# Kernel tuning notes

Hardware: AMD Instinct MI355X
Metric: run time of the kernel (lower is better)

Reference implementation:

```python
import jax, jax.numpy as jnp
import numpy as np

D_MODEL = 768
D_FF = 3072
N_BEHAVIORS = 4
EPS = 1e-12


def layer_norm(x, g, b):
    m = jnp.mean(x, axis=-1, keepdims=True)
    v = jnp.mean(jnp.square(x - m), axis=-1, keepdims=True)
    return (x - m) * jax.lax.rsqrt(v + EPS) * g + b


def setup_inputs() -> dict:
    key = jax.random.key(0)
    ks = jax.random.split(key, 8)
    B, L = 8, 2048
    s1 = 1.0 / np.sqrt(D_MODEL)
    s2 = 1.0 / np.sqrt(D_FF)
    return {
        "input_tensor": jax.random.normal(ks[0], (B, L, D_MODEL), dtype=jnp.float32),
        "type_seq": jax.random.randint(ks[1], (B, L), 0, N_BEHAVIORS + 1),
        # per-behavior FeedForward params, stacked on leading n dim
        "W1": jax.random.normal(ks[2], (N_BEHAVIORS, D_MODEL, D_FF), dtype=jnp.float32) * s1,
        "b1": jnp.zeros((N_BEHAVIORS, D_FF), dtype=jnp.float32),
        "W2": jax.random.normal(ks[3], (N_BEHAVIORS, D_FF, D_MODEL), dtype=jnp.float32) * s2,
        "b2": jnp.zeros((N_BEHAVIORS, D_MODEL), dtype=jnp.float32),
        "ln_g": jnp.ones((N_BEHAVIORS, D_MODEL), dtype=jnp.float32),
        "ln_b": jnp.zeros((N_BEHAVIORS, D_MODEL), dtype=jnp.float32),
        # outer LayerNorm params
        "out_g": jnp.ones((D_MODEL,), dtype=jnp.float32),
        "out_b": jnp.zeros((D_MODEL,), dtype=jnp.float32),
    }


def reference(input_tensor, type_seq, W1, b1, W2, b2, ln_g, ln_b, out_g, out_b):
    n = W1.shape[0]
    # run every behavior's FeedForward over the full sequence (dense over-compute)
    h = jnp.einsum('BLH,nHF->nBLF', input_tensor, W1) + b1[:, None, None, :]
    h = jax.nn.gelu(h, approximate=False)  # torch 'gelu' = exact erf form
    h = jnp.einsum('nBLF,nFH->nBLH', h, W2) + b2[:, None, None, :]
    # per-expert residual LayerNorm (FeedForward with residual=True)
    h = layer_norm(h + input_tensor[None], ln_g[:, None, None, :], ln_b[:, None, None, :])
    # prepend zeros branch (class 0 = padding) then one-hot select per token
    stacked = jnp.concatenate([jnp.zeros_like(input_tensor)[None], h], axis=0)  # [n+1,B,L,H]
    onehot = jax.nn.one_hot(type_seq, n + 1, dtype=input_tensor.dtype)  # [B,L,n+1]
    sel = jnp.einsum('nBLH,BLn->BLH', stacked, onehot)
    # dropout is identity in eval; fused residual + LayerNorm
    return layer_norm(sel + input_tensor, out_g, out_b)
```

## Files before the change

### kernel.cpp

```cpp
#include <hip/hip_runtime.h>
#include <hip/hip_bf16.h>
#include <math.h>

#define NTOK   16384
#define DM     768
#define DF     3072
#define NEXP   4

#define RBLKS  64
#define XBLKS  768
#define WBLKS  288
#define PREP_BLKS (RBLKS + XBLKS + 2 * WBLKS)

typedef short bf16x8 __attribute__((ext_vector_type(8)));
typedef float f32x4  __attribute__((ext_vector_type(4)));

#define WS_CNT    0u
#define WS_BASES  256u
#define WS_POS    512u
#define WS_LIST   (512u + 65536u)
#define WS_XB     (WS_LIST + 262144u)
#define WS_W1T    (WS_XB + 25165824u)
#define WS_W2T    (WS_W1T + 18874368u)
#define WS_H1     (WS_W2T + 18874368u)
#define WS_H2     (WS_H1 + 100663296u)
#define WS_END    (WS_H2 + 25165824u)

__device__ __forceinline__ ushort f2bf(float f) {
    unsigned int v; __builtin_memcpy(&v, &f, 4);
    v = v + 0x7fffu + ((v >> 16) & 1u);
    return (ushort)(v >> 16);
}
__device__ __forceinline__ float bf2f(ushort u) {
    unsigned int v = ((unsigned int)u) << 16;
    float f; __builtin_memcpy(&f, &v, 4); return f;
}

__device__ __forceinline__ float fast_gelu(float v) {
    float y = v + 0.044715f * v * v * v;
    float e = __builtin_amdgcn_exp2f(-2.3022082f * y);
    return v * __builtin_amdgcn_rcpf(1.0f + e);
}

typedef __attribute__((address_space(1))) const void gvoid_t;
typedef __attribute__((address_space(3))) void lvoid_t;
__device__ __forceinline__ void cp16(const void* g, void* l) {
    __builtin_amdgcn_global_load_lds((gvoid_t*)g, (lvoid_t*)l, 16, 0, 0);
}

__device__ __forceinline__ int xcd_remap(int id, int T) {
    const int q = T >> 3, r = T & 7;
    const int x = id & 7, j = id >> 3;
    return (x < r ? x * (q + 1) : r * (q + 1) + (x - r) * q) + j;
}

__device__ __forceinline__ void transpose_tile(
    const float* __restrict__ src, ushort* __restrict__ dst, int R, int C,
    int bx, int by, int tid, ushort* tile ) {
    const int r0 = by * 64, c0 = bx * 64;
#pragma unroll
    for (int q = 0; q < 2; ++q) {
        int li = q * 256 + tid;
        int r = li >> 3, c = (li & 7) * 8;
        const float* s = src + (size_t)(r0 + r) * C + (c0 + c);
        float4 v0 = *(const float4*)s;
        float4 v1 = *(const float4*)(s + 4);
        ushort tmp[8];
        tmp[0] = f2bf(v0.x); tmp[1] = f2bf(v0.y); tmp[2] = f2bf(v0.z); tmp[3] = f2bf(v0.w);
        tmp[4] = f2bf(v1.x); tmp[5] = f2bf(v1.y); tmp[6] = f2bf(v1.z); tmp[7] = f2bf(v1.w);
        int sw = (((c >> 3) ^ ((r >> 3) & 7)) << 3);
        *(uint4*)&tile[r * 72 + sw] = *(uint4*)tmp;
    }
    __syncthreads();
#pragma unroll
    for (int q = 0; q < 2; ++q) {
        int li = q * 256 + tid;
        int r = li >> 3, c = (li & 7) * 8;
        ushort tmp[8];
#pragma unroll
        for (int j = 0; j < 8; ++j)
            tmp[j] = tile[(c + j) * 72 +
                          ((((r >> 3) & 7) ^ (((c + j) >> 3) & 7)) << 3) + (r & 7)];
        *(uint4*)(dst + (size_t)(c0 + r) * R + (r0 + c)) = *(uint4*)tmp;
    }
}

__global__ __launch_bounds__(256) void prep_kernel(
    const int* __restrict__ type_seq, const float* __restrict__ X,
    const float* __restrict__ W1, const float* __restrict__ W2,
    int* __restrict__ cnt,
    int* __restrict__ pos_of, int* __restrict__ list,
    ushort* __restrict__ Xb, ushort* __restrict__ W1t, ushort* __restrict__ W2t) {
    __shared__ ushort tile[64 * 72];
    __shared__ int lcnt[NEXP];
    __shared__ int lbase[NEXP];
    const int tid = threadIdx.x;
    const int bid = blockIdx.x;

    if (bid < RBLKS) {
        if (tid < NEXP) lcnt[tid] = 0;
        __syncthreads();
        const int lane = tid & 63;
        const int t = bid * 256 + tid;
        const int k = type_seq[t];
        int my_e = -1, my_p = 0;
#pragma unroll
        for (int e = 0; e < NEXP; ++e) {
            unsigned long long m = __ballot(k == e + 1);
            int total = __popcll(m);
            int b = 0;
            if (lane == 0 && total) b = atomicAdd(&lcnt[e], total);
            b = __shfl(b, 0, 64);
            if (k == e + 1) {
                my_e = e;
                my_p = b + __popcll(m & ((1ull << lane) - 1ull));
            }
        }
        __syncthreads();
        if (tid < NEXP && lcnt[tid] > 0)
            lbase[tid] = atomicAdd(&cnt[tid], lcnt[tid]);
        __syncthreads();
        if (my_e >= 0) {
            int gp = lbase[my_e] + my_p;
            list[my_e * NTOK + gp] = t;
            pos_of[t] = gp;
        }
        return;
    }

    int id = bid - RBLKS;
    if (id < XBLKS) {
        size_t ibase = ((size_t)id * 8 * 256 + tid) * 8;
        float4 va[8], vb[8];
#pragma unroll
        for (int k = 0; k < 8; ++k) {
            va[k] = *(const float4*)(X + ibase + (size_t)k * 2048);
            vb[k] = *(const float4*)(X + ibase + (size_t)k * 2048 + 4);
        }
#pragma unroll
        for (int k = 0; k < 8; ++k) {
            ushort tmp[8];
            tmp[0] = f2bf(va[k].x); tmp[1] = f2bf(va[k].y);
            tmp[2] = f2bf(va[k].z); tmp[3] = f2bf(va[k].w);
            tmp[4] = f2bf(vb[k].x); tmp[5] = f2bf(vb[k].y);
            tmp[6] = f2bf(vb[k].z); tmp[7] = f2bf(vb[k].w);
            *(uint4*)(Xb + ibase + (size_t)k * 2048) = *(uint4*)tmp;
        }
        return;
    }
    id -= XBLKS;
    if (id < WBLKS) {
#pragma unroll 1
        for (int k = 0; k < 8; ++k) {
            int tt = id * 8 + k;
            int z = tt / 576, rr = tt % 576;
            size_t mb = (size_t)z * DM * DF;
            transpose_tile(W1 + mb, W1t + mb, DM, DF, rr % 48, rr / 48, tid, tile);
            __syncthreads();
        }
        return;
    }
    id -= WBLKS;
    {
#pragma unroll 1
        for (int k = 0; k < 8; ++k) {
            int tt = id * 8 + k;
            int z = tt / 576, rr = tt % 576;
            size_t mb = (size_t)z * DF * DM;
            transpose_tile(W2 + mb, W2t + mb, DF, DM, rr % 12, rr / 12, tid, tile);
            __syncthreads();
        }
    }
}

__global__ __launch_bounds__(64) void scan_kernel(
    const int* __restrict__ cnt, int* __restrict__ bases) {
    if (threadIdx.x == 0) {
        int s = 0, mb = 0;
        for (int e = 0; e < NEXP; ++e) {
            bases[e] = s;
            bases[8 + e] = mb;
            s += cnt[e];
            mb += (cnt[e] + 127) >> 7;
        }
        bases[12] = mb;
    }
}


__global__ __launch_bounds__(512, 4) void gemm1_kernel(
    const ushort* __restrict__ Xb, const ushort* __restrict__ W1t,
    const float* __restrict__ b1, const int* __restrict__ cnt,
    const int* __restrict__ bases, const int* __restrict__ list,
    ushort* __restrict__ h1) {
    const int mb = bases[12];
    const int T = mb * 12;
    int id = blockIdx.y * 12 + blockIdx.x;
    if (id >= T) return;
    id = xcd_remap(id, T);
    const int y = id / 12;
    const int n0 = (id % 12) * 256;
    const int* mboff = bases + 8;
    const int e = (y >= mboff[1]) + (y >= mboff[2]) + (y >= mboff[3]);
    const int m0 = (y - mboff[e]) << 7;
    const int count = cnt[e];
    const int NK = DM / 32;

    __shared__ __align__(16) short As[3][4096];
    __shared__ __align__(16) short Bs[3][8192];

    const int tid = threadIdx.x;
    const int wave = tid >> 6, lane = tid & 63;
    const int wm = (wave & 1) * 64, wn = (wave >> 1) * 64;
    const int lrow = lane & 15;
    const int qg = lane >> 4;

    const int srow = tid >> 2;
    const int qsrc = ((tid & 3) ^ ((tid >> 3) & 3)) * 8;
    int r0 = min(m0 + srow, count - 1);
    const ushort* a0 = Xb + (size_t)list[e * NTOK + r0] * DM + qsrc;
    const ushort* Wb = W1t + (size_t)e * DF * DM;
    const ushort* bp0 = Wb + (size_t)(n0 + srow) * DM + qsrc;
    const ushort* bp1 = bp0 + (size_t)128 * DM;

    int aOff[4], bOff[4];
#pragma unroll
    for (int i = 0; i < 4; ++i) {
        int ra = wm + i * 16 + lrow;
        aOff[i] = ra * 32 + (qg ^ ((ra >> 1) & 3)) * 8;
        int rb = wn + i * 16 + lrow;
        bOff[i] = rb * 32 + (qg ^ ((rb >> 1) & 3)) * 8;
    }

    f32x4 z = {0.f, 0.f, 0.f, 0.f};
    f32x4 acc[4][4];
#pragma unroll
    for (int i = 0; i < 4; ++i)
#pragma unroll
        for (int j = 0; j < 4; ++j) acc[i][j] = z;

    auto STAGE = [&](int wb) {
        cp16(a0, &As[wb][0] + tid * 8);
        cp16(bp0, &Bs[wb][0] + tid * 8);
        cp16(bp1, &Bs[wb][4096] + tid * 8);
        a0 += 32; bp0 += 32; bp1 += 32;
    };

    STAGE(0); STAGE(1);
    int rb = 0;
    for (int ks = 0; ks < NK; ++ks) {
        __builtin_amdgcn_sched_barrier(0);
        if (ks + 1 < NK) { asm volatile("s_waitcnt vmcnt(3)" ::: "memory"); }
        else             { asm volatile("s_waitcnt vmcnt(0)" ::: "memory"); }
        __builtin_amdgcn_s_barrier();
        __builtin_amdgcn_sched_barrier(0);
        if (ks + 2 < NK) {
            int wb = rb - 1; if (wb < 0) wb += 3;
            STAGE(wb);
        }
        const short* Ab = &As[rb][0];
        const short* Bb = &Bs[rb][0];
        bf16x8 av[4], bv[4];
#pragma unroll
        for (int i = 0; i < 4; ++i) av[i] = *(const bf16x8*)(Ab + aOff[i]);
#pragma unroll
        for (int j = 0; j < 4; ++j) bv[j] = *(const bf16x8*)(Bb + bOff[j]);
#pragma unroll
        for (int i = 0; i < 4; ++i)
#pragma unroll
            for (int j = 0; j < 4; ++j)
                acc[i][j] = __builtin_amdgcn_mfma_f32_16x16x32_bf16(av[i], bv[j], acc[i][j], 0, 0, 0);
        rb = (rb + 1 == 3) ? 0 : rb + 1;
    }

    const int base = bases[e];
    float bias[4];
#pragma unroll
    for (int j = 0; j < 4; ++j)
        bias[j] = b1[e * DF + n0 + wn + j * 16 + lrow];
#pragma unroll
    for (int i = 0; i < 4; ++i) {
        int gm = m0 + wm + i * 16 + qg * 4;
#pragma unroll
        for (int j = 0; j < 4; ++j) {
            int gn = n0 + wn + j * 16 + lrow;
#pragma unroll
            for (int r = 0; r < 4; ++r) {
                int row = gm + r;
                if (row < count) {
                    float v = acc[i][j][r] + bias[j];
                    h1[(size_t)(base + row) * DF + gn] = f2bf(fast_gelu(v));
                }
            }
        }
    }
}

__global__ __launch_bounds__(256, 3) void gemm2_kernel(
    const ushort* __restrict__ h1, const ushort* __restrict__ W2t,
    const float* __restrict__ b2, const int* __restrict__ cnt,
    const int* __restrict__ bases, ushort* __restrict__ h2) {
    const int mb = bases[12];
    const int T = mb * 6;
    int id = blockIdx.y * 6 + blockIdx.x;
    if (id >= T) return;
    id = xcd_remap(id, T);
    const int y = id / 6;
    const int n0 = (id % 6) * 128;
    const int* mboff = bases + 8;
    const int e = (y >= mboff[1]) + (y >= mboff[2]) + (y >= mboff[3]);
    const int m0 = (y - mboff[e]) << 7;
    const int count = cnt[e];
    const int base = bases[e];
    const int NK = DF / 32;

    __shared__ __align__(16) short As[3][4096];
    __shared__ __align__(16) short Bs[3][4096];

    const int tid = threadIdx.x;
    const int wave = tid >> 6, lane = tid & 63;
    const int wm = (wave & 1) * 64, wn = (wave >> 1) * 64;
    const int lrow = lane & 15;
    const int qg = lane >> 4;

    const int srow = tid >> 2;
    const int qsrc = ((tid & 3) ^ ((tid >> 3) & 3)) * 8;
    int r0 = min(m0 + srow, count - 1);
    int r1 = min(m0 + 64 + srow, count - 1);
    const ushort* a0 = h1 + (size_t)(base + r0) * DF + qsrc;
    const ushort* a1 = h1 + (size_t)(base + r1) * DF + qsrc;
    const ushort* Wb = W2t + (size_t)e * DM * DF;
    const ushort* bp0 = Wb + (size_t)(n0 + srow) * DF + qsrc;
    const ushort* bp1 = bp0 + (size_t)64 * DF;

    int aOff[4], bOff[4];
#pragma unroll
    for (int i = 0; i < 4; ++i) {
        int ra = wm + i * 16 + lrow;
        aOff[i] = ra * 32 + (qg ^ ((ra >> 1) & 3)) * 8;
        int rbo = wn + i * 16 + lrow;
        bOff[i] = rbo * 32 + (qg ^ ((rbo >> 1) & 3)) * 8;
    }

    f32x4 z = {0.f, 0.f, 0.f, 0.f};
    f32x4 acc[4][4];
#pragma unroll
    for (int i = 0; i < 4; ++i)
#pragma unroll
        for (int j = 0; j < 4; ++j) acc[i][j] = z;

    auto STAGE = [&](int wb) {
        cp16(a0, &As[wb][0] + tid * 8);
        cp16(a1, &As[wb][2048] + tid * 8);
        cp16(bp0, &Bs[wb][0] + tid * 8);
        cp16(bp1, &Bs[wb][2048] + tid * 8);
        a0 += 32; a1 += 32; bp0 += 32; bp1 += 32;
    };

    STAGE(0); STAGE(1);
    int rb = 0;
    for (int ks = 0; ks < NK; ++ks) {
        __builtin_amdgcn_sched_barrier(0);
        if (ks + 1 < NK) { asm volatile("s_waitcnt vmcnt(4)" ::: "memory"); }
        else             { asm volatile("s_waitcnt vmcnt(0)" ::: "memory"); }
        __builtin_amdgcn_s_barrier();
        __builtin_amdgcn_sched_barrier(0);
        if (ks + 2 < NK) {
            int wb = rb - 1; if (wb < 0) wb += 3;
            STAGE(wb);
        }
        const short* Ab = &As[rb][0];
        const short* Bb = &Bs[rb][0];
        bf16x8 av[4], bv[4];
#pragma unroll
        for (int i = 0; i < 4; ++i) av[i] = *(const bf16x8*)(Ab + aOff[i]);
#pragma unroll
        for (int j = 0; j < 4; ++j) bv[j] = *(const bf16x8*)(Bb + bOff[j]);
#pragma unroll
        for (int i = 0; i < 4; ++i)
#pragma unroll
            for (int j = 0; j < 4; ++j)
                acc[i][j] = __builtin_amdgcn_mfma_f32_16x16x32_bf16(av[i], bv[j], acc[i][j], 0, 0, 0);
        rb = (rb + 1 == 3) ? 0 : rb + 1;
    }

    float bias[4];
#pragma unroll
    for (int j = 0; j < 4; ++j)
        bias[j] = b2[e * DM + n0 + wn + j * 16 + lrow];
#pragma unroll
    for (int i = 0; i < 4; ++i) {
        int gm = m0 + wm + i * 16 + qg * 4;
#pragma unroll
        for (int j = 0; j < 4; ++j) {
            int gn = n0 + wn + j * 16 + lrow;
#pragma unroll
            for (int r = 0; r < 4; ++r) {
                int row = gm + r;
                if (row < count)
                    h2[(size_t)(base + row) * DM + gn] = f2bf(acc[i][j][r] + bias[j]);
            }
        }
    }
}

__global__ __launch_bounds__(256) void finalize_kernel(
    const float* __restrict__ X, const int* __restrict__ type_seq,
    const int* __restrict__ pos_of, const int* __restrict__ bases,
    const ushort* __restrict__ h2,
    const float* __restrict__ ln_g, const float* __restrict__ ln_b,
    const float* __restrict__ out_g, const float* __restrict__ out_b,
    float* __restrict__ out) {
    const int tid = threadIdx.x;
    const int wave = tid >> 6, lane = tid & 63;
    const int col0 = lane * 4;

#pragma unroll 1
    for (int ti = 0; ti < 2; ++ti) {
        const int t = blockIdx.x * 8 + wave * 2 + ti;
        const int k = type_seq[t];

        const float* Xr = X + (size_t)t * DM;
        float4 xv[3];
#pragma unroll
        for (int j = 0; j < 3; ++j) xv[j] = *(const float4*)(Xr + col0 + j * 256);

        float rv[12];
        if (k > 0) {
            const int e = k - 1;
            const size_t row = (size_t)(bases[e] + pos_of[t]);
            const ushort* hr = h2 + row * DM;
            float v[12];
            float s1 = 0.f, s2 = 0.f;
#pragma unroll
            for (int j = 0; j < 3; ++j) {
                ushort4 hv = *(const ushort4*)(hr + col0 + j * 256);
                float f0 = bf2f(hv.x) + xv[j].x;
                float f1 = bf2f(hv.y) + xv[j].y;
                float f2 = bf2f(hv.z) + xv[j].z;
                float f3 = bf2f(hv.w) + xv[j].w;
                v[j * 4 + 0] = f0; v[j * 4 + 1] = f1;
                v[j * 4 + 2] = f2; v[j * 4 + 3] = f3;
                s1 += (f0 + f1) + (f2 + f3);
                s2 += (f0 * f0 + f1 * f1) + (f2 * f2 + f3 * f3);
            }
#pragma unroll
            for (int off = 32; off > 0; off >>= 1) {
                s1 += __shfl_xor(s1, off, 64);
                s2 += __shfl_xor(s2, off, 64);
            }
            float m = s1 * (1.f / DM);
            float inv = rsqrtf(s2 * (1.f / DM) - m * m + 1e-12f);
#pragma unroll
            for (int j = 0; j < 3; ++j) {
                float4 g = *(const float4*)(ln_g + e * DM + col0 + j * 256);
                float4 b = *(const float4*)(ln_b + e * DM + col0 + j * 256);
                rv[j * 4 + 0] = (v[j * 4 + 0] - m) * inv * g.x + b.x;
                rv[j * 4 + 1] = (v[j * 4 + 1] - m) * inv * g.y + b.y;
                rv[j * 4 + 2] = (v[j * 4 + 2] - m) * inv * g.z + b.z;
                rv[j * 4 + 3] = (v[j * 4 + 3] - m) * inv * g.w + b.w;
            }
        } else {
#pragma unroll
            for (int j = 0; j < 12; ++j) rv[j] = 0.f;
        }

        float w[12];
        float s1 = 0.f, s2 = 0.f;
#pragma unroll
        for (int j = 0; j < 3; ++j) {
            float f0 = rv[j * 4 + 0] + xv[j].x;
            float f1 = rv[j * 4 + 1] + xv[j].y;
            float f2 = rv[j * 4 + 2] + xv[j].z;
            float f3 = rv[j * 4 + 3] + xv[j].w;
            w[j * 4 + 0] = f0; w[j * 4 + 1] = f1;
            w[j * 4 + 2] = f2; w[j * 4 + 3] = f3;
            s1 += (f0 + f1) + (f2 + f3);
            s2 += (f0 * f0 + f1 * f1) + (f2 * f2 + f3 * f3);
        }
#pragma unroll
        for (int off = 32; off > 0; off >>= 1) {
            s1 += __shfl_xor(s1, off, 64);
            s2 += __shfl_xor(s2, off, 64);
        }
        float m = s1 * (1.f / DM);
        float inv = rsqrtf(s2 * (1.f / DM) - m * m + 1e-12f);
#pragma unroll
        for (int j = 0; j < 3; ++j) {
            float4 g = *(const float4*)(out_g + col0 + j * 256);
            float4 b = *(const float4*)(out_b + col0 + j * 256);
            float4 o;
            o.x = (w[j * 4 + 0] - m) * inv * g.x + b.x;
            o.y = (w[j * 4 + 1] - m) * inv * g.y + b.y;
            o.z = (w[j * 4 + 2] - m) * inv * g.z + b.z;
            o.w = (w[j * 4 + 3] - m) * inv * g.w + b.w;
            *(float4*)(out + (size_t)t * DM + col0 + j * 256) = o;
        }
    }
}

extern "C" void kernel_launch(void* const* d_in, const int* in_sizes, int n_in,
                              void* d_out, int out_size, void* d_ws, size_t ws_size,
                              hipStream_t stream) {
    if (ws_size < (size_t)WS_END) return;

    const float* X     = (const float*)d_in[0];
    const int*   type  = (const int*)d_in[1];
    const float* W1    = (const float*)d_in[2];
    const float* b1    = (const float*)d_in[3];
    const float* W2    = (const float*)d_in[4];
    const float* b2    = (const float*)d_in[5];
    const float* ln_g  = (const float*)d_in[6];
    const float* ln_b  = (const float*)d_in[7];
    const float* out_g = (const float*)d_in[8];
    const float* out_b = (const float*)d_in[9];
    float* out = (float*)d_out;

    char* ws = (char*)d_ws;
    int* cnt    = (int*)(ws + WS_CNT);
    int* bases  = (int*)(ws + WS_BASES);
    int* pos_of = (int*)(ws + WS_POS);
    int* list   = (int*)(ws + WS_LIST);
    ushort* Xb  = (ushort*)(ws + WS_XB);
    ushort* W1t = (ushort*)(ws + WS_W1T);
    ushort* W2t = (ushort*)(ws + WS_W2T);
    ushort* h1  = (ushort*)(ws + WS_H1);
    ushort* h2  = (ushort*)(ws + WS_H2);

    hipMemsetAsync(cnt, 0, NEXP * sizeof(int), stream);
    prep_kernel<<<PREP_BLKS, 256, 0, stream>>>(type, X, W1, W2,
                                               cnt, pos_of, list, Xb, W1t, W2t);
    scan_kernel<<<1, 64, 0, stream>>>(cnt, bases);
    gemm1_kernel<<<dim3(12, 132), 512, 0, stream>>>(Xb, W1t, b1, cnt, bases, list, h1);
    gemm2_kernel<<<dim3(6, 132), 256, 0, stream>>>(h1, W2t, b2, cnt, bases, h2);
    finalize_kernel<<<NTOK / 8, 256, 0, stream>>>(X, type, pos_of, bases, h2, ln_g, ln_b, out_g, out_b, out);
}
```

Measured before the change: 379.0 us.

## Enlarge gemm1 tile to 256x256 and double-buffer weight transpose loads

Gemm1 now processes 256-row M tiles per block (8 waves as 2x4, each 128x64), halving the number of M blocks. This raises operand reuse per LDS stage. The scan kernel emits separate block offsets for gemm1 (256-row) and gemm2 (128-row). The weight transpose in prep now prefetches the next tile's global loads into registers while the current tile is written through a double-buffered LDS tile, overlapping load latency with the shuffle. The larger accumulator set increases register pressure, and occupancy hint drops to 2 blocks per CU.

```diff
diff --git a/kernel.cpp b/kernel.cpp
--- a/kernel.cpp
+++ b/kernel.cpp
@@ -54,44 +54,13 @@
     return (x < r ? x * (q + 1) : r * (q + 1) + (x - r) * q) + j;
 }
 
-__device__ __forceinline__ void transpose_tile(
-    const float* __restrict__ src, ushort* __restrict__ dst, int R, int C,
-    int bx, int by, int tid, ushort* tile ) {
-    const int r0 = by * 64, c0 = bx * 64;
-#pragma unroll
-    for (int q = 0; q < 2; ++q) {
-        int li = q * 256 + tid;
-        int r = li >> 3, c = (li & 7) * 8;
-        const float* s = src + (size_t)(r0 + r) * C + (c0 + c);
-        float4 v0 = *(const float4*)s;
-        float4 v1 = *(const float4*)(s + 4);
-        ushort tmp[8];
-        tmp[0] = f2bf(v0.x); tmp[1] = f2bf(v0.y); tmp[2] = f2bf(v0.z); tmp[3] = f2bf(v0.w);
-        tmp[4] = f2bf(v1.x); tmp[5] = f2bf(v1.y); tmp[6] = f2bf(v1.z); tmp[7] = f2bf(v1.w);
-        int sw = (((c >> 3) ^ ((r >> 3) & 7)) << 3);
-        *(uint4*)&tile[r * 72 + sw] = *(uint4*)tmp;
-    }
-    __syncthreads();
-#pragma unroll
-    for (int q = 0; q < 2; ++q) {
-        int li = q * 256 + tid;
-        int r = li >> 3, c = (li & 7) * 8;
-        ushort tmp[8];
-#pragma unroll
-        for (int j = 0; j < 8; ++j)
-            tmp[j] = tile[(c + j) * 72 +
-                          ((((r >> 3) & 7) ^ (((c + j) >> 3) & 7)) << 3) + (r & 7)];
-        *(uint4*)(dst + (size_t)(c0 + r) * R + (r0 + c)) = *(uint4*)tmp;
-    }
-}
-
 __global__ __launch_bounds__(256) void prep_kernel(
     const int* __restrict__ type_seq, const float* __restrict__ X,
     const float* __restrict__ W1, const float* __restrict__ W2,
     int* __restrict__ cnt,
     int* __restrict__ pos_of, int* __restrict__ list,
     ushort* __restrict__ Xb, ushort* __restrict__ W1t, ushort* __restrict__ W2t) {
-    __shared__ ushort tile[64 * 72];
+    __shared__ ushort tbuf[2][64 * 72];
     __shared__ int lcnt[NEXP];
     __shared__ int lbase[NEXP];
     const int tid = threadIdx.x;
@@ -149,26 +118,91 @@
         return;
     }
     id -= XBLKS;
+
+    const int lr = tid >> 3;
+    const int lc = (tid & 7) * 8;
+    float4 v[2][2];
+
     if (id < WBLKS) {
+        const int base_tt = id * 8;
+        auto LOADT = [&](int tt) {
+            int z = tt / 576, rr = tt % 576, bx = rr % 48, by = rr / 48;
+            const float* s0 = W1 + (size_t)z * DM * DF + (size_t)(by * 64 + lr) * DF + bx * 64 + lc;
+            v[0][0] = *(const float4*)s0;       v[0][1] = *(const float4*)(s0 + 4);
+            const float* s1 = s0 + (size_t)32 * DF;
+            v[1][0] = *(const float4*)s1;       v[1][1] = *(const float4*)(s1 + 4);
+        };
+        LOADT(base_tt);
 #pragma unroll 1
         for (int k = 0; k < 8; ++k) {
-            int tt = id * 8 + k;
-            int z = tt / 576, rr = tt % 576;
-            size_t mb = (size_t)z * DM * DF;
-            transpose_tile(W1 + mb, W1t + mb, DM, DF, rr % 48, rr / 48, tid, tile);
+            ushort* tb = &tbuf[k & 1][0];
+#pragma unroll
+            for (int q = 0; q < 2; ++q) {
+                int r = lr + q * 32;
+                ushort tmp[8];
+                tmp[0] = f2bf(v[q][0].x); tmp[1] = f2bf(v[q][0].y);
+                tmp[2] = f2bf(v[q][0].z); tmp[3] = f2bf(v[q][0].w);
+                tmp[4] = f2bf(v[q][1].x); tmp[5] = f2bf(v[q][1].y);
+                tmp[6] = f2bf(v[q][1].z); tmp[7] = f2bf(v[q][1].w);
+                int sw = (((lc >> 3) ^ ((r >> 3) & 7)) << 3);
+                *(uint4*)&tb[r * 72 + sw] = *(uint4*)tmp;
+            }
+            if (k < 7) LOADT(base_tt + k + 1);
             __syncthreads();
+            int tt = base_tt + k;
+            int z = tt / 576, rr = tt % 576, bx = rr % 48, by = rr / 48;
+#pragma unroll
+            for (int q = 0; q < 2; ++q) {
+                int r = lr + q * 32;
+                ushort tmp[8];
+#pragma unroll
+                for (int j = 0; j < 8; ++j)
+                    tmp[j] = tb[(lc + j) * 72 +
+                                ((((r >> 3) & 7) ^ (((lc + j) >> 3) & 7)) << 3) + (r & 7)];
+                *(uint4*)(W1t + (size_t)z * DM * DF + (size_t)(bx * 64 + r) * DM + by * 64 + lc) = *(uint4*)tmp;
+            }
         }
         return;
     }
     id -= WBLKS;
     {
+        const int base_tt = id * 8;
+        auto LOADT = [&](int tt) {
+            int z = tt / 576, rr = tt % 576, bx = rr % 12, by = rr / 12;
+            const float* s0 = W2 + (size_t)z * DM * DF + (size_t)(by * 64 + lr) * DM + bx * 64 + lc;
+            v[0][0] = *(const float4*)s0;       v[0][1] = *(const float4*)(s0 + 4);
+            const float* s1 = s0 + (size_t)32 * DM;
+            v[1][0] = *(const float4*)s1;       v[1][1] = *(const float4*)(s1 + 4);
+        };
+        LOADT(base_tt);
 #pragma unroll 1
         for (int k = 0; k < 8; ++k) {
-            int tt = id * 8 + k;
-            int z = tt / 576, rr = tt % 576;
-            size_t mb = (size_t)z * DF * DM;
-            transpose_tile(W2 + mb, W2t + mb, DF, DM, rr % 12, rr / 12, tid, tile);
+            ushort* tb = &tbuf[k & 1][0];
+#pragma unroll
+            for (int q = 0; q < 2; ++q) {
+                int r = lr + q * 32;
+                ushort tmp[8];
+                tmp[0] = f2bf(v[q][0].x); tmp[1] = f2bf(v[q][0].y);
+                tmp[2] = f2bf(v[q][0].z); tmp[3] = f2bf(v[q][0].w);
+                tmp[4] = f2bf(v[q][1].x); tmp[5] = f2bf(v[q][1].y);
+                tmp[6] = f2bf(v[q][1].z); tmp[7] = f2bf(v[q][1].w);
+                int sw = (((lc >> 3) ^ ((r >> 3) & 7)) << 3);
+                *(uint4*)&tb[r * 72 + sw] = *(uint4*)tmp;
+            }
+            if (k < 7) LOADT(base_tt + k + 1);
             __syncthreads();
+            int tt = base_tt + k;
+            int z = tt / 576, rr = tt % 576, bx = rr % 12, by = rr / 12;
+#pragma unroll
+            for (int q = 0; q < 2; ++q) {
+                int r = lr + q * 32;
+                ushort tmp[8];
+#pragma unroll
+                for (int j = 0; j < 8; ++j)
+                    tmp[j] = tb[(lc + j) * 72 +
+                                ((((r >> 3) & 7) ^ (((lc + j) >> 3) & 7)) << 3) + (r & 7)];
+                *(uint4*)(W2t + (size_t)z * DM * DF + (size_t)(bx * 64 + r) * DF + by * 64 + lc) = *(uint4*)tmp;
+            }
         }
     }
 }
@@ -176,19 +210,21 @@
 __global__ __launch_bounds__(64) void scan_kernel(
     const int* __restrict__ cnt, int* __restrict__ bases) {
     if (threadIdx.x == 0) {
-        int s = 0, mb = 0;
+        int s = 0, mb2 = 0, mb1 = 0;
         for (int e = 0; e < NEXP; ++e) {
             bases[e] = s;
-            bases[8 + e] = mb;
+            bases[8 + e] = mb2;
+            bases[16 + e] = mb1;
             s += cnt[e];
-            mb += (cnt[e] + 127) >> 7;
-        }
-        bases[12] = mb;
-    }
-}
-
-
-__global__ __launch_bounds__(512, 4) void gemm1_kernel(
+            mb2 += (cnt[e] + 255) >> 8;
+            mb1 += (cnt[e] + 127) >> 7;
+        }
+        bases[12] = mb2;
+        bases[20] = mb1;
+    }
+}
+
+__global__ __launch_bounds__(512, 2) void gemm1_kernel(
     const ushort* __restrict__ Xb, const ushort* __restrict__ W1t,
     const float* __restrict__ b1, const int* __restrict__ cnt,
     const int* __restrict__ bases, const int* __restrict__ list,
@@ -202,158 +238,53 @@
     const int n0 = (id % 12) * 256;
     const int* mboff = bases + 8;
     const int e = (y >= mboff[1]) + (y >= mboff[2]) + (y >= mboff[3]);
-    const int m0 = (y - mboff[e]) << 7;
+    const int m0 = (y - mboff[e]) << 8;
     const int count = cnt[e];
     const int NK = DM / 32;
 
-    __shared__ __align__(16) short As[3][4096];
+    __shared__ __align__(16) short As[3][8192];
     __shared__ __align__(16) short Bs[3][8192];
 
     const int tid = threadIdx.x;
     const int wave = tid >> 6, lane = tid & 63;
-    const int wm = (wave & 1) * 64, wn = (wave >> 1) * 64;
+    const int wm = (wave >> 2) * 128, wn = (wave & 3) * 64;
     const int lrow = lane & 15;
     const int qg = lane >> 4;
 
     const int srow = tid >> 2;
     const int qsrc = ((tid & 3) ^ ((tid >> 3) & 3)) * 8;
     int r0 = min(m0 + srow, count - 1);
+    int r1 = min(m0 + srow + 128, count - 1);
     const ushort* a0 = Xb + (size_t)list[e * NTOK + r0] * DM + qsrc;
+    const ushort* a1 = Xb + (size_t)list[e * NTOK + r1] * DM + qsrc;
     const ushort* Wb = W1t + (size_t)e * DF * DM;
     const ushort* bp0 = Wb + (size_t)(n0 + srow) * DM + qsrc;
     const ushort* bp1 = bp0 + (size_t)128 * DM;
 
-    int aOff[4], bOff[4];
-#pragma unroll
-    for (int i = 0; i < 4; ++i) {
+    int aOff[8], bOff[4];
+#pragma unroll
+    for (int i = 0; i < 8; ++i) {
         int ra = wm + i * 16 + lrow;
         aOff[i] = ra * 32 + (qg ^ ((ra >> 1) & 3)) * 8;
-        int rb = wn + i * 16 + lrow;
-        bOff[i] = rb * 32 + (qg ^ ((rb >> 1) & 3)) * 8;
+    }
+#pragma unroll
+    for (int j = 0; j < 4; ++j) {
+        int rb = wn + j * 16 + lrow;
+        bOff[j] = rb * 32 + (qg ^ ((rb >> 1) & 3)) * 8;
     }
 
     f32x4 z = {0.f, 0.f, 0.f, 0.f};
-    f32x4 acc[4][4];
-#pragma unroll
-    for (int i = 0; i < 4; ++i)
+    f32x4 acc[8][4];
+#pragma unroll
+    for (int i = 0; i < 8; ++i)
 #pragma unroll
         for (int j = 0; j < 4; ++j) acc[i][j] = z;
 
     auto STAGE = [&](int wb) {
         cp16(a0, &As[wb][0] + tid * 8);
+        cp16(a1, &As[wb][4096] + tid * 8);
         cp16(bp0, &Bs[wb][0] + tid * 8);
         cp16(bp1, &Bs[wb][4096] + tid * 8);
-        a0 += 32; bp0 += 32; bp1 += 32;
-    };
-
-    STAGE(0); STAGE(1);
-    int rb = 0;
-    for (int ks = 0; ks < NK; ++ks) {
-        __builtin_amdgcn_sched_barrier(0);
-        if (ks + 1 < NK) { asm volatile("s_waitcnt vmcnt(3)" ::: "memory"); }
-        else             { asm volatile("s_waitcnt vmcnt(0)" ::: "memory"); }
-        __builtin_amdgcn_s_barrier();
-        __builtin_amdgcn_sched_barrier(0);
-        if (ks + 2 < NK) {
-            int wb = rb - 1; if (wb < 0) wb += 3;
-            STAGE(wb);
-        }
-        const short* Ab = &As[rb][0];
-        const short* Bb = &Bs[rb][0];
-        bf16x8 av[4], bv[4];
-#pragma unroll
-        for (int i = 0; i < 4; ++i) av[i] = *(const bf16x8*)(Ab + aOff[i]);
-#pragma unroll
-        for (int j = 0; j < 4; ++j) bv[j] = *(const bf16x8*)(Bb + bOff[j]);
-#pragma unroll
-        for (int i = 0; i < 4; ++i)
-#pragma unroll
-            for (int j = 0; j < 4; ++j)
-                acc[i][j] = __builtin_amdgcn_mfma_f32_16x16x32_bf16(av[i], bv[j], acc[i][j], 0, 0, 0);
-        rb = (rb + 1 == 3) ? 0 : rb + 1;
-    }
-
-    const int base = bases[e];
-    float bias[4];
-#pragma unroll
-    for (int j = 0; j < 4; ++j)
-        bias[j] = b1[e * DF + n0 + wn + j * 16 + lrow];
-#pragma unroll
-    for (int i = 0; i < 4; ++i) {
-        int gm = m0 + wm + i * 16 + qg * 4;
-#pragma unroll
-        for (int j = 0; j < 4; ++j) {
-            int gn = n0 + wn + j * 16 + lrow;
-#pragma unroll
-            for (int r = 0; r < 4; ++r) {
-                int row = gm + r;
-                if (row < count) {
-                    float v = acc[i][j][r] + bias[j];
-                    h1[(size_t)(base + row) * DF + gn] = f2bf(fast_gelu(v));
-                }
-            }
-        }
-    }
-}
-
-__global__ __launch_bounds__(256, 3) void gemm2_kernel(
-    const ushort* __restrict__ h1, const ushort* __restrict__ W2t,
-    const float* __restrict__ b2, const int* __restrict__ cnt,
-    const int* __restrict__ bases, ushort* __restrict__ h2) {
-    const int mb = bases[12];
-    const int T = mb * 6;
-    int id = blockIdx.y * 6 + blockIdx.x;
-    if (id >= T) return;
-    id = xcd_remap(id, T);
-    const int y = id / 6;
-    const int n0 = (id % 6) * 128;
-    const int* mboff = bases + 8;
-    const int e = (y >= mboff[1]) + (y >= mboff[2]) + (y >= mboff[3]);
-    const int m0 = (y - mboff[e]) << 7;
-    const int count = cnt[e];
-    const int base = bases[e];
-    const int NK = DF / 32;
-
-    __shared__ __align__(16) short As[3][4096];
-    __shared__ __align__(16) short Bs[3][4096];
-
-    const int tid = threadIdx.x;
-    const int wave = tid >> 6, lane = tid & 63;
-    const int wm = (wave & 1) * 64, wn = (wave >> 1) * 64;
-    const int lrow = lane & 15;
-    const int qg = lane >> 4;
-
-    const int srow = tid >> 2;
-    const int qsrc = ((tid & 3) ^ ((tid >> 3) & 3)) * 8;
-    int r0 = min(m0 + srow, count - 1);
-    int r1 = min(m0 + 64 + srow, count - 1);
-    const ushort* a0 = h1 + (size_t)(base + r0) * DF + qsrc;
-    const ushort* a1 = h1 + (size_t)(base + r1) * DF + qsrc;
-    const ushort* Wb = W2t + (size_t)e * DM * DF;
-    const ushort* bp0 = Wb + (size_t)(n0 + srow) * DF + qsrc;
-    const ushort* bp1 = bp0 + (size_t)64 * DF;
-
-    int aOff[4], bOff[4];
-#pragma unroll
-    for (int i = 0; i < 4; ++i) {
-        int ra = wm + i * 16 + lrow;
-        aOff[i] = ra * 32 + (qg ^ ((ra >> 1) & 3)) * 8;
-        int rbo = wn + i * 16 + lrow;
-        bOff[i] = rbo * 32 + (qg ^ ((rbo >> 1) & 3)) * 8;
-    }
-
-    f32x4 z = {0.f, 0.f, 0.f, 0.f};
-    f32x4 acc[4][4];
-#pragma unroll
-    for (int i = 0; i < 4; ++i)
-#pragma unroll
-        for (int j = 0; j < 4; ++j) acc[i][j] = z;
-
-    auto STAGE = [&](int wb) {
-        cp16(a0, &As[wb][0] + tid * 8);
-        cp16(a1, &As[wb][2048] + tid * 8);
-        cp16(bp0, &Bs[wb][0] + tid * 8);
-        cp16(bp1, &Bs[wb][2048] + tid * 8);
         a0 += 32; a1 += 32; bp0 += 32; bp1 += 32;
     };
 
@@ -371,6 +302,117 @@
         }
         const short* Ab = &As[rb][0];
         const short* Bb = &Bs[rb][0];
+        bf16x8 av[8], bv[4];
+#pragma unroll
+        for (int i = 0; i < 8; ++i) av[i] = *(const bf16x8*)(Ab + aOff[i]);
+#pragma unroll
+        for (int j = 0; j < 4; ++j) bv[j] = *(const bf16x8*)(Bb + bOff[j]);
+#pragma unroll
+        for (int i = 0; i < 8; ++i)
+#pragma unroll
+            for (int j = 0; j < 4; ++j)
+                acc[i][j] = __builtin_amdgcn_mfma_f32_16x16x32_bf16(av[i], bv[j], acc[i][j], 0, 0, 0);
+        rb = (rb + 1 == 3) ? 0 : rb + 1;
+    }
+
+    const int base = bases[e];
+    float bias[4];
+#pragma unroll
+    for (int j = 0; j < 4; ++j)
+        bias[j] = b1[e * DF + n0 + wn + j * 16 + lrow];
+#pragma unroll
+    for (int i = 0; i < 8; ++i) {
+        int gm = m0 + wm + i * 16 + qg * 4;
+#pragma unroll
+        for (int j = 0; j < 4; ++j) {
+            int gn = n0 + wn + j * 16 + lrow;
+#pragma unroll
+            for (int r = 0; r < 4; ++r) {
+                int row = gm + r;
+                if (row < count) {
+                    float v = acc[i][j][r] + bias[j];
+                    h1[(size_t)(base + row) * DF + gn] = f2bf(fast_gelu(v));
+                }
+            }
+        }
+    }
+}
+
+__global__ __launch_bounds__(256, 3) void gemm2_kernel(
+    const ushort* __restrict__ h1, const ushort* __restrict__ W2t,
+    const float* __restrict__ b2, const int* __restrict__ cnt,
+    const int* __restrict__ bases, ushort* __restrict__ h2) {
+    const int mb = bases[20];
+    const int T = mb * 6;
+    int id = blockIdx.y * 6 + blockIdx.x;
+    if (id >= T) return;
+    id = xcd_remap(id, T);
+    const int y = id / 6;
+    const int n0 = (id % 6) * 128;
+    const int* mboff = bases + 16;
+    const int e = (y >= mboff[1]) + (y >= mboff[2]) + (y >= mboff[3]);
+    const int m0 = (y - mboff[e]) << 7;
+    const int count = cnt[e];
+    const int base = bases[e];
+    const int NK = DF / 32;
+
+    __shared__ __align__(16) short As[3][4096];
+    __shared__ __align__(16) short Bs[3][4096];
+
+    const int tid = threadIdx.x;
+    const int wave = tid >> 6, lane = tid & 63;
+    const int wm = (wave & 1) * 64, wn = (wave >> 1) * 64;
+    const int lrow = lane & 15;
+    const int qg = lane >> 4;
+
+    const int srow = tid >> 2;
+    const int qsrc = ((tid & 3) ^ ((tid >> 3) & 3)) * 8;
+    int r0 = min(m0 + srow, count - 1);
+    int r1 = min(m0 + 64 + srow, count - 1);
+    const ushort* a0 = h1 + (size_t)(base + r0) * DF + qsrc;
+    const ushort* a1 = h1 + (size_t)(base + r1) * DF + qsrc;
+    const ushort* Wb = W2t + (size_t)e * DM * DF;
+    const ushort* bp0 = Wb + (size_t)(n0 + srow) * DF + qsrc;
+    const ushort* bp1 = bp0 + (size_t)64 * DF;
+
+    int aOff[4], bOff[4];
+#pragma unroll
+    for (int i = 0; i < 4; ++i) {
+        int ra = wm + i * 16 + lrow;
+        aOff[i] = ra * 32 + (qg ^ ((ra >> 1) & 3)) * 8;
+        int rbo = wn + i * 16 + lrow;
+        bOff[i] = rbo * 32 + (qg ^ ((rbo >> 1) & 3)) * 8;
+    }
+
+    f32x4 z = {0.f, 0.f, 0.f, 0.f};
+    f32x4 acc[4][4];
+#pragma unroll
+    for (int i = 0; i < 4; ++i)
+#pragma unroll
+        for (int j = 0; j < 4; ++j) acc[i][j] = z;
+
+    auto STAGE = [&](int wb) {
+        cp16(a0, &As[wb][0] + tid * 8);
+        cp16(a1, &As[wb][2048] + tid * 8);
+        cp16(bp0, &Bs[wb][0] + tid * 8);
+        cp16(bp1, &Bs[wb][2048] + tid * 8);
+        a0 += 32; a1 += 32; bp0 += 32; bp1 += 32;
+    };
+
+    STAGE(0); STAGE(1);
+    int rb = 0;
+    for (int ks = 0; ks < NK; ++ks) {
+        __builtin_amdgcn_sched_barrier(0);
+        if (ks + 1 < NK) { asm volatile("s_waitcnt vmcnt(4)" ::: "memory"); }
+        else             { asm volatile("s_waitcnt vmcnt(0)" ::: "memory"); }
+        __builtin_amdgcn_s_barrier();
+        __builtin_amdgcn_sched_barrier(0);
+        if (ks + 2 < NK) {
+            int wb = rb - 1; if (wb < 0) wb += 3;
+            STAGE(wb);
+        }
+        const short* Ab = &As[rb][0];
+        const short* Bb = &Bs[rb][0];
         bf16x8 av[4], bv[4];
 #pragma unroll
         for (int i = 0; i < 4; ++i) av[i] = *(const bf16x8*)(Ab + aOff[i]);
@@ -531,7 +573,7 @@
     prep_kernel<<<PREP_BLKS, 256, 0, stream>>>(type, X, W1, W2,
                                                cnt, pos_of, list, Xb, W1t, W2t);
     scan_kernel<<<1, 64, 0, stream>>>(cnt, bases);
-    gemm1_kernel<<<dim3(12, 132), 512, 0, stream>>>(Xb, W1t, b1, cnt, bases, list, h1);
+    gemm1_kernel<<<dim3(12, 68), 512, 0, stream>>>(Xb, W1t, b1, cnt, bases, list, h1);
     gemm2_kernel<<<dim3(6, 132), 256, 0, stream>>>(h1, W2t, b2, cnt, bases, h2);
     finalize_kernel<<<NTOK / 8, 256, 0, stream>>>(X, type, pos_of, bases, h2, ln_g, ln_b, out_g, out_b, out);
 }
```

Result: slower. 417.3 us (+10.1%).
